# Performance work log

Measured on AMD Instinct MI355X. Metric: run time of the kernel, lower is better.

## Reference

```python
import jax, jax.numpy as jnp
from jax import lax
import numpy as np

EPS = 1e-6


def _conv1d_same(x, w, pad):
    # x: [B, 1, L], w: [1, 1, K]; XLA conv is cross-correlation, matching nn.Conv1d.
    return lax.conv_general_dilated(
        x, w, window_strides=(1,), padding=[(pad, pad)],
        dimension_numbers=("NCH", "OIH", "NCH"))


def setup_inputs() -> dict:
    key = jax.random.key(0)
    k_m, = jax.random.split(key, 1)
    B, L, K, NUM_LAYERS = 4096, 8192, 31, 10
    m = jax.random.uniform(k_m, (B, L), dtype=jnp.float32)
    # Gaussian instrument PSF (sigma=5), normalized to unit sum.
    xs = jnp.arange(K, dtype=jnp.float32) - (K - 1) / 2.0
    psf = jnp.exp(-(xs ** 2) / (2.0 * 5.0 ** 2))
    psf = psf / jnp.sum(psf)
    alpha = jnp.ones((NUM_LAYERS,), dtype=jnp.float32)
    return {"m": m, "psf": psf, "alpha": alpha}


def reference(m, psf, alpha):
    K = psf.shape[0]
    pad = (K - 1) // 2
    w = psf.reshape(1, 1, K)          # conv weight (PSF)
    w_flip = w[:, :, ::-1]             # flipped-PSF weight
    x = m[:, None, :]                  # [B, 1, L]
    s0 = jnp.full_like(x, 0.5)

    def step(s, a):
        s_conv = _conv1d_same(s, w, pad) + EPS
        ratio = x / s_conv
        correction = _conv1d_same(ratio, w_flip, pad) + EPS
        correction = jnp.maximum(correction, EPS)
        s = jnp.maximum(s * correction ** a, EPS)
        return s, None

    s, _ = lax.scan(step, s0, alpha)
    return s[:, 0, :]
```

## Files before the change

kernel.cpp:

```cpp
#include <hip/hip_runtime.h>
#include <math.h>

#define EPS     1e-6f
#define LROW    8192
#define NLAYER  10
#define NT      512

#define HBUF    16448
#define FRONTE  16
#define SCALE_F   2048.0f
#define INV_SCALE 4.8828125e-4f

typedef _Float16 half8  __attribute__((ext_vector_type(8)));
typedef __fp16   fp16x2 __attribute__((ext_vector_type(2)));
typedef float    f32x4  __attribute__((ext_vector_type(4)));

union H8U { uint4 u; half8 h; };
union H2U { fp16x2 h; unsigned int u; };

__device__ __forceinline__ half8 ldfrag(const char* p) {
    H8U w; w.u = *(const uint4*)(p); return w.h;
}

__device__ __forceinline__ int swz(int a) { return a ^ ((a >> 3) & 0x70); }

struct HL { _Float16 h, l; };
__device__ __forceinline__ HL fsplit(float v) {
    HL r;
    r.h = (_Float16)v;
    r.l = (_Float16)((v - (float)r.h) * SCALE_F);
    return r;
}

__device__ __forceinline__ float sgpr_f(float v) {
    return __int_as_float(__builtin_amdgcn_readfirstlane(__float_as_int(v)));
}

__device__ __forceinline__ void build_w(const float* wl, int am, int ag,
        half8& h01, half8& l01, half8& h2z, half8& l2z)
{
#pragma unroll
    for (int j = 0; j < 8; ++j) {
        const int k   = 8 * ag + j;
        const int i01 = k - am - 1;
        HL a = fsplit(wl[i01 + 16]);
        h01[j] = a.h; l01[j] = a.l;
        float v2 = 0.0f;
        if (k < 16) v2 = wl[31 + k - am + 16];
        HL b = fsplit(v2);
        h2z[j] = b.h; l2z[j] = b.l;
    }
}

__device__ __forceinline__ f32x4 conv_tile(const char* ph, const char* pl,
        int o01, int o2, half8 hA01, half8 lA01, half8 hA2, half8 lA2)
{
    half8 hS01 = ldfrag(ph + o01);
    half8 lS01 = ldfrag(pl + o01);
    half8 hS2  = ldfrag(ph + o2);
    half8 lS2  = ldfrag(pl + o2);
    f32x4 H  = {EPS, EPS, EPS, EPS};
    f32x4 L1 = {0.0f, 0.0f, 0.0f, 0.0f};
    f32x4 L2 = {0.0f, 0.0f, 0.0f, 0.0f};
    H  = __builtin_amdgcn_mfma_f32_16x16x32_f16(hA01, hS01, H,  0, 0, 0);
    H  = __builtin_amdgcn_mfma_f32_16x16x32_f16(hA2,  hS2,  H,  0, 0, 0);
    L1 = __builtin_amdgcn_mfma_f32_16x16x32_f16(lA01, hS01, L1, 0, 0, 0);
    L1 = __builtin_amdgcn_mfma_f32_16x16x32_f16(hA01, lS01, L1, 0, 0, 0);
    L2 = __builtin_amdgcn_mfma_f32_16x16x32_f16(lA2,  hS2,  L2, 0, 0, 0);
    L2 = __builtin_amdgcn_mfma_f32_16x16x32_f16(hA2,  lS2,  L2, 0, 0, 0);
    f32x4 r;
#pragma unroll
    for (int i = 0; i < 4; ++i) r[i] = fmaf(L1[i] + L2[i], INV_SCALE, H[i]);
    return r;
}

__global__ __launch_bounds__(NT, 4) void drl_kernel(
    const float* __restrict__ m,
    const float* __restrict__ psf,
    const float* __restrict__ alpha,
    float* __restrict__ out)
{
    __shared__ __align__(16) char lds[4 * HBUF + 256];
    char* SBh = lds;
    char* SBl = lds + HBUF;
    char* RBh = lds + 2 * HBUF;
    char* RBl = lds + 3 * HBUF;
    float* wl = (float*)(lds + 4 * HBUF);

    const int t    = threadIdx.x;
    const int lane = t & 63;
    const int wid  = t >> 6;
    const int am   = lane & 15;
    const int ag   = lane >> 4;
    const int row  = blockIdx.x;
    const float* mrow = m + (size_t)row * LROW;
    float*       orow = out + (size_t)row * LROW;

    {
        const uint4 z4 = make_uint4(0u, 0u, 0u, 0u);
        uint4* z = (uint4*)lds;
#pragma unroll
        for (int k = 0; k < 9; ++k) {
            int i = t + NT * k;
            if (i < 4112) z[i] = z4;
        }
        if (t < 64) wl[t] = (t >= 16 && t <= 46) ? psf[t - 16] : 0.0f;
    }
    __syncthreads();

    {
        const uint4 p5 = make_uint4(0x38003800u, 0x38003800u, 0x38003800u, 0x38003800u);
        int a = swz(32 + 32 * t);
        *(uint4*)(SBh + a)      = p5;
        *(uint4*)(SBh + a + 16) = p5;
    }
    __syncthreads();

    half8 hA01, lA01, hA2, lA2;
    build_w(wl, am, ag, hA01, lA01, hA2, lA2);

    const int n0 = 64 * wid;
    const int xoff = 16 * (n0 + am) + 4 * ag;
    float4 xr[4];
#pragma unroll
    for (int c = 0; c < 4; ++c)
        xr[c] = *(const float4*)(mrow + xoff + 256 * c);

    float sreg[16];
#pragma unroll
    for (int i = 0; i < 16; ++i) sreg[i] = 0.5f;

    int rb01[4], rb2[4], wbw[4];
#pragma unroll
    for (int c = 0; c < 4; ++c) {
        const int e01 = 16 * (n0 + am - 1) + 8 * ag       + FRONTE + 256 * c;
        const int e2  = 16 * (n0 + am + 1) + 8 * (ag & 1) + FRONTE + 256 * c;
        const int ew  = 16 * (n0 + am)     + 4 * ag       + FRONTE + 256 * c;
        rb01[c] = swz(2 * e01);
        rb2[c]  = swz(2 * e2);
        wbw[c]  = swz(2 * ew);
    }

#pragma unroll 1
    for (int layer = 0; layer < NLAYER; ++layer) {
        const float a = sgpr_f(alpha[layer]);

#pragma unroll
        for (int c = 0; c < 4; ++c) {
            f32x4 acc = conv_tile(SBh, SBl, rb01[c], rb2[c],
                                  hA01, lA01, hA2, lA2);
            const float4 xv = xr[c];
            float r0 = xv.x * __builtin_amdgcn_rcpf(acc[0]);
            float r1 = xv.y * __builtin_amdgcn_rcpf(acc[1]);
            float r2 = xv.z * __builtin_amdgcn_rcpf(acc[2]);
            float r3 = xv.w * __builtin_amdgcn_rcpf(acc[3]);
            H2U hA, hB, lA, lB;
            hA.h = __builtin_amdgcn_cvt_pkrtz(r0, r1);
            hB.h = __builtin_amdgcn_cvt_pkrtz(r2, r3);
            float d0 = (r0 - (float)hA.h.x) * SCALE_F;
            float d1 = (r1 - (float)hA.h.y) * SCALE_F;
            float d2 = (r2 - (float)hB.h.x) * SCALE_F;
            float d3 = (r3 - (float)hB.h.y) * SCALE_F;
            lA.h = __builtin_amdgcn_cvt_pkrtz(d0, d1);
            lB.h = __builtin_amdgcn_cvt_pkrtz(d2, d3);
            *(uint2*)(RBh + wbw[c]) = make_uint2(hA.u, hB.u);
            *(uint2*)(RBl + wbw[c]) = make_uint2(lA.u, lB.u);
        }
        __syncthreads();

#pragma unroll
        for (int c = 0; c < 4; ++c) {
            f32x4 acc = conv_tile(RBh, RBl, rb01[c], rb2[c],
                                  hA01, lA01, hA2, lA2);
            float c0 = fmaxf(acc[0], EPS);
            float c1 = fmaxf(acc[1], EPS);
            float c2 = fmaxf(acc[2], EPS);
            float c3 = fmaxf(acc[3], EPS);
            if (a != 1.0f) {
                c0 = powf(c0, a); c1 = powf(c1, a);
                c2 = powf(c2, a); c3 = powf(c3, a);
            }
            float s0 = fmaxf(sreg[4*c+0] * c0, EPS);
            float s1 = fmaxf(sreg[4*c+1] * c1, EPS);
            float s2 = fmaxf(sreg[4*c+2] * c2, EPS);
            float s3 = fmaxf(sreg[4*c+3] * c3, EPS);
            sreg[4*c+0] = s0; sreg[4*c+1] = s1;
            sreg[4*c+2] = s2; sreg[4*c+3] = s3;
            H2U hA, hB, lA, lB;
            hA.h = __builtin_amdgcn_cvt_pkrtz(s0, s1);
            hB.h = __builtin_amdgcn_cvt_pkrtz(s2, s3);
            float d0 = (s0 - (float)hA.h.x) * SCALE_F;
            float d1 = (s1 - (float)hA.h.y) * SCALE_F;
            float d2 = (s2 - (float)hB.h.x) * SCALE_F;
            float d3 = (s3 - (float)hB.h.y) * SCALE_F;
            lA.h = __builtin_amdgcn_cvt_pkrtz(d0, d1);
            lB.h = __builtin_amdgcn_cvt_pkrtz(d2, d3);
            *(uint2*)(SBh + wbw[c]) = make_uint2(hA.u, hB.u);
            *(uint2*)(SBl + wbw[c]) = make_uint2(lA.u, lB.u);
        }
        __syncthreads();
    }

#pragma unroll
    for (int c = 0; c < 4; ++c) {
        *(float4*)(orow + xoff + 256 * c) =
            make_float4(sreg[4*c], sreg[4*c+1], sreg[4*c+2], sreg[4*c+3]);
    }
}

extern "C" void kernel_launch(void* const* d_in, const int* in_sizes, int n_in,
                              void* d_out, int out_size, void* d_ws, size_t ws_size,
                              hipStream_t stream) {
    const float* m     = (const float*)d_in[0];
    const float* psf   = (const float*)d_in[1];
    const float* alpha = (const float*)d_in[2];
    float* out = (float*)d_out;
    const int B = in_sizes[0] / LROW;
    drl_kernel<<<dim3(B), dim3(NT), 0, stream>>>(m, psf, alpha, out);
}
```

Before: 426.8 us.

## Switch banded convolution from 16x16x32 to 32x32x16 MFMA tiles

Replaces the per-chunk 16x16x32 MFMA Toeplitz formulation (six MFMAs per 16x16 tile, split into 01 and 2 weight blocks) with 32x32x16 MFMAs. Each lane's column now covers 32 contiguous outputs, with four K-chunks of weight fragments. The LDS layout, read/write offsets and input/output indexing are reworked to match. The aim is to cut MFMA issue count and wasted zero-weight work per output. The cost is larger accumulators (three f32x16) and more weight-fragment registers, which may hurt occupancy.

```diff
diff --git a/kernel.cpp b/kernel.cpp
--- a/kernel.cpp
+++ b/kernel.cpp
@@ -7,13 +7,12 @@
 #define NT      512
 
 #define HBUF    16448
-#define FRONTE  16
 #define SCALE_F   2048.0f
 #define INV_SCALE 4.8828125e-4f
 
 typedef _Float16 half8  __attribute__((ext_vector_type(8)));
 typedef __fp16   fp16x2 __attribute__((ext_vector_type(2)));
-typedef float    f32x4  __attribute__((ext_vector_type(4)));
+typedef float    f32x16 __attribute__((ext_vector_type(16)));
 
 union H8U { uint4 u; half8 h; };
 union H2U { fp16x2 h; unsigned int u; };
@@ -36,62 +35,25 @@
     return __int_as_float(__builtin_amdgcn_readfirstlane(__float_as_int(v)));
 }
 
-__device__ __forceinline__ void build_w(const float* wl, int am, int ag,
-        half8& h01, half8& l01, half8& h2z, half8& l2z)
-{
-#pragma unroll
-    for (int j = 0; j < 8; ++j) {
-        const int k   = 8 * ag + j;
-        const int i01 = k - am - 1;
-        HL a = fsplit(wl[i01 + 16]);
-        h01[j] = a.h; l01[j] = a.l;
-        float v2 = 0.0f;
-        if (k < 16) v2 = wl[31 + k - am + 16];
-        HL b = fsplit(v2);
-        h2z[j] = b.h; l2z[j] = b.l;
-    }
-}
-
-__device__ __forceinline__ f32x4 conv_tile(const char* ph, const char* pl,
-        int o01, int o2, half8 hA01, half8 lA01, half8 hA2, half8 lA2)
-{
-    half8 hS01 = ldfrag(ph + o01);
-    half8 lS01 = ldfrag(pl + o01);
-    half8 hS2  = ldfrag(ph + o2);
-    half8 lS2  = ldfrag(pl + o2);
-    f32x4 H  = {EPS, EPS, EPS, EPS};
-    f32x4 L1 = {0.0f, 0.0f, 0.0f, 0.0f};
-    f32x4 L2 = {0.0f, 0.0f, 0.0f, 0.0f};
-    H  = __builtin_amdgcn_mfma_f32_16x16x32_f16(hA01, hS01, H,  0, 0, 0);
-    H  = __builtin_amdgcn_mfma_f32_16x16x32_f16(hA2,  hS2,  H,  0, 0, 0);
-    L1 = __builtin_amdgcn_mfma_f32_16x16x32_f16(lA01, hS01, L1, 0, 0, 0);
-    L1 = __builtin_amdgcn_mfma_f32_16x16x32_f16(hA01, lS01, L1, 0, 0, 0);
-    L2 = __builtin_amdgcn_mfma_f32_16x16x32_f16(lA2,  hS2,  L2, 0, 0, 0);
-    L2 = __builtin_amdgcn_mfma_f32_16x16x32_f16(hA2,  lS2,  L2, 0, 0, 0);
-    f32x4 r;
-#pragma unroll
-    for (int i = 0; i < 4; ++i) r[i] = fmaf(L1[i] + L2[i], INV_SCALE, H[i]);
-    return r;
-}
-
 __global__ __launch_bounds__(NT, 4) void drl_kernel(
     const float* __restrict__ m,
     const float* __restrict__ psf,
     const float* __restrict__ alpha,
     float* __restrict__ out)
 {
-    __shared__ __align__(16) char lds[4 * HBUF + 256];
+    __shared__ __align__(16) char lds[4 * HBUF + 384];
     char* SBh = lds;
     char* SBl = lds + HBUF;
     char* RBh = lds + 2 * HBUF;
     char* RBl = lds + 3 * HBUF;
-    float* wl = (float*)(lds + 4 * HBUF);
+    float* wl2 = (float*)(lds + 4 * HBUF);
 
     const int t    = threadIdx.x;
     const int lane = t & 63;
     const int wid  = t >> 6;
-    const int am   = lane & 15;
-    const int ag   = lane >> 4;
+    const int aj   = lane & 31;
+    const int h    = lane >> 5;
+    const int col  = 32 * wid + aj;
     const int row  = blockIdx.x;
     const float* mrow = m + (size_t)row * LROW;
     float*       orow = out + (size_t)row * LROW;
@@ -104,107 +66,136 @@
             int i = t + NT * k;
             if (i < 4112) z[i] = z4;
         }
-        if (t < 64) wl[t] = (t >= 16 && t <= 46) ? psf[t - 16] : 0.0f;
+        if (t < 96) wl2[t] = (t >= 32 && t <= 62) ? psf[t - 32] : 0.0f;
     }
     __syncthreads();
 
     {
         const uint4 p5 = make_uint4(0x38003800u, 0x38003800u, 0x38003800u, 0x38003800u);
-        int a = swz(32 + 32 * t);
-        *(uint4*)(SBh + a)      = p5;
-        *(uint4*)(SBh + a + 16) = p5;
+        int a0 = swz(32 * t + 32);
+        *(uint4*)(SBh + a0) = p5;
+        int a1 = swz(32 * t + 48);
+        *(uint4*)(SBh + a1) = p5;
     }
     __syncthreads();
 
-    half8 hA01, lA01, hA2, lA2;
-    build_w(wl, am, ag, hA01, lA01, hA2, lA2);
-
-    const int n0 = 64 * wid;
-    const int xoff = 16 * (n0 + am) + 4 * ag;
-    float4 xr[4];
-#pragma unroll
-    for (int c = 0; c < 4; ++c)
-        xr[c] = *(const float4*)(mrow + xoff + 256 * c);
+    half8 hA[4], lA[4];
+#pragma unroll
+    for (int c = 0; c < 4; ++c) {
+#pragma unroll
+        for (int j = 0; j < 8; ++j) {
+            HL w = fsplit(wl2[16 * c + 8 * h + j - aj + 31]);
+            hA[c][j] = w.h; lA[c][j] = w.l;
+        }
+    }
+
+    int rb[4], wb[4];
+#pragma unroll
+    for (int c = 0; c < 4; ++c) {
+        rb[c] = swz(64 * col + 32 * c + 16 * h);
+        wb[c] = swz(64 * col + 16 * c + 8 * h + 32);
+    }
+
+    float xr[16];
+#pragma unroll
+    for (int q = 0; q < 4; ++q) {
+        float4 v = *(const float4*)(mrow + 32 * col + 8 * q + 4 * h);
+        xr[4*q+0] = v.x; xr[4*q+1] = v.y; xr[4*q+2] = v.z; xr[4*q+3] = v.w;
+    }
 
     float sreg[16];
 #pragma unroll
     for (int i = 0; i < 16; ++i) sreg[i] = 0.5f;
-
-    int rb01[4], rb2[4], wbw[4];
-#pragma unroll
-    for (int c = 0; c < 4; ++c) {
-        const int e01 = 16 * (n0 + am - 1) + 8 * ag       + FRONTE + 256 * c;
-        const int e2  = 16 * (n0 + am + 1) + 8 * (ag & 1) + FRONTE + 256 * c;
-        const int ew  = 16 * (n0 + am)     + 4 * ag       + FRONTE + 256 * c;
-        rb01[c] = swz(2 * e01);
-        rb2[c]  = swz(2 * e2);
-        wbw[c]  = swz(2 * ew);
-    }
 
 #pragma unroll 1
     for (int layer = 0; layer < NLAYER; ++layer) {
-        const float a = sgpr_f(alpha[layer]);
-
-#pragma unroll
-        for (int c = 0; c < 4; ++c) {
-            f32x4 acc = conv_tile(SBh, SBl, rb01[c], rb2[c],
-                                  hA01, lA01, hA2, lA2);
-            const float4 xv = xr[c];
-            float r0 = xv.x * __builtin_amdgcn_rcpf(acc[0]);
-            float r1 = xv.y * __builtin_amdgcn_rcpf(acc[1]);
-            float r2 = xv.z * __builtin_amdgcn_rcpf(acc[2]);
-            float r3 = xv.w * __builtin_amdgcn_rcpf(acc[3]);
-            H2U hA, hB, lA, lB;
-            hA.h = __builtin_amdgcn_cvt_pkrtz(r0, r1);
-            hB.h = __builtin_amdgcn_cvt_pkrtz(r2, r3);
-            float d0 = (r0 - (float)hA.h.x) * SCALE_F;
-            float d1 = (r1 - (float)hA.h.y) * SCALE_F;
-            float d2 = (r2 - (float)hB.h.x) * SCALE_F;
-            float d3 = (r3 - (float)hB.h.y) * SCALE_F;
-            lA.h = __builtin_amdgcn_cvt_pkrtz(d0, d1);
-            lB.h = __builtin_amdgcn_cvt_pkrtz(d2, d3);
-            *(uint2*)(RBh + wbw[c]) = make_uint2(hA.u, hB.u);
-            *(uint2*)(RBl + wbw[c]) = make_uint2(lA.u, lB.u);
+        const float av = sgpr_f(alpha[layer]);
+
+        {
+            f32x16 H, L1, L2;
+#pragma unroll
+            for (int i = 0; i < 16; ++i) { H[i] = EPS; L1[i] = 0.0f; L2[i] = 0.0f; }
+#pragma unroll
+            for (int c = 0; c < 4; ++c) {
+                half8 hB = ldfrag(SBh + rb[c]);
+                half8 lB = ldfrag(SBl + rb[c]);
+                H  = __builtin_amdgcn_mfma_f32_32x32x16_f16(hA[c], hB, H,  0, 0, 0);
+                L1 = __builtin_amdgcn_mfma_f32_32x32x16_f16(lA[c], hB, L1, 0, 0, 0);
+                L2 = __builtin_amdgcn_mfma_f32_32x32x16_f16(hA[c], lB, L2, 0, 0, 0);
+            }
+#pragma unroll
+            for (int q = 0; q < 4; ++q) {
+                float a0 = fmaf(L1[4*q+0] + L2[4*q+0], INV_SCALE, H[4*q+0]);
+                float a1 = fmaf(L1[4*q+1] + L2[4*q+1], INV_SCALE, H[4*q+1]);
+                float a2 = fmaf(L1[4*q+2] + L2[4*q+2], INV_SCALE, H[4*q+2]);
+                float a3 = fmaf(L1[4*q+3] + L2[4*q+3], INV_SCALE, H[4*q+3]);
+                float r0 = xr[4*q+0] * __builtin_amdgcn_rcpf(a0);
+                float r1 = xr[4*q+1] * __builtin_amdgcn_rcpf(a1);
+                float r2 = xr[4*q+2] * __builtin_amdgcn_rcpf(a2);
+                float r3 = xr[4*q+3] * __builtin_amdgcn_rcpf(a3);
+                H2U hP, hQ, lP, lQ;
+                hP.h = __builtin_amdgcn_cvt_pkrtz(r0, r1);
+                hQ.h = __builtin_amdgcn_cvt_pkrtz(r2, r3);
+                float d0 = (r0 - (float)hP.h.x) * SCALE_F;
+                float d1 = (r1 - (float)hP.h.y) * SCALE_F;
+                float d2 = (r2 - (float)hQ.h.x) * SCALE_F;
+                float d3 = (r3 - (float)hQ.h.y) * SCALE_F;
+                lP.h = __builtin_amdgcn_cvt_pkrtz(d0, d1);
+                lQ.h = __builtin_amdgcn_cvt_pkrtz(d2, d3);
+                *(uint2*)(RBh + wb[q]) = make_uint2(hP.u, hQ.u);
+                *(uint2*)(RBl + wb[q]) = make_uint2(lP.u, lQ.u);
+            }
         }
         __syncthreads();
 
-#pragma unroll
-        for (int c = 0; c < 4; ++c) {
-            f32x4 acc = conv_tile(RBh, RBl, rb01[c], rb2[c],
-                                  hA01, lA01, hA2, lA2);
-            float c0 = fmaxf(acc[0], EPS);
-            float c1 = fmaxf(acc[1], EPS);
-            float c2 = fmaxf(acc[2], EPS);
-            float c3 = fmaxf(acc[3], EPS);
-            if (a != 1.0f) {
-                c0 = powf(c0, a); c1 = powf(c1, a);
-                c2 = powf(c2, a); c3 = powf(c3, a);
-            }
-            float s0 = fmaxf(sreg[4*c+0] * c0, EPS);
-            float s1 = fmaxf(sreg[4*c+1] * c1, EPS);
-            float s2 = fmaxf(sreg[4*c+2] * c2, EPS);
-            float s3 = fmaxf(sreg[4*c+3] * c3, EPS);
-            sreg[4*c+0] = s0; sreg[4*c+1] = s1;
-            sreg[4*c+2] = s2; sreg[4*c+3] = s3;
-            H2U hA, hB, lA, lB;
-            hA.h = __builtin_amdgcn_cvt_pkrtz(s0, s1);
-            hB.h = __builtin_amdgcn_cvt_pkrtz(s2, s3);
-            float d0 = (s0 - (float)hA.h.x) * SCALE_F;
-            float d1 = (s1 - (float)hA.h.y) * SCALE_F;
-            float d2 = (s2 - (float)hB.h.x) * SCALE_F;
-            float d3 = (s3 - (float)hB.h.y) * SCALE_F;
-            lA.h = __builtin_amdgcn_cvt_pkrtz(d0, d1);
-            lB.h = __builtin_amdgcn_cvt_pkrtz(d2, d3);
-            *(uint2*)(SBh + wbw[c]) = make_uint2(hA.u, hB.u);
-            *(uint2*)(SBl + wbw[c]) = make_uint2(lA.u, lB.u);
+        {
+            f32x16 H, L1, L2;
+#pragma unroll
+            for (int i = 0; i < 16; ++i) { H[i] = EPS; L1[i] = 0.0f; L2[i] = 0.0f; }
+#pragma unroll
+            for (int c = 0; c < 4; ++c) {
+                half8 hB = ldfrag(RBh + rb[c]);
+                half8 lB = ldfrag(RBl + rb[c]);
+                H  = __builtin_amdgcn_mfma_f32_32x32x16_f16(hA[c], hB, H,  0, 0, 0);
+                L1 = __builtin_amdgcn_mfma_f32_32x32x16_f16(lA[c], hB, L1, 0, 0, 0);
+                L2 = __builtin_amdgcn_mfma_f32_32x32x16_f16(hA[c], lB, L2, 0, 0, 0);
+            }
+#pragma unroll
+            for (int q = 0; q < 4; ++q) {
+                float c0 = fmaxf(fmaf(L1[4*q+0] + L2[4*q+0], INV_SCALE, H[4*q+0]), EPS);
+                float c1 = fmaxf(fmaf(L1[4*q+1] + L2[4*q+1], INV_SCALE, H[4*q+1]), EPS);
+                float c2 = fmaxf(fmaf(L1[4*q+2] + L2[4*q+2], INV_SCALE, H[4*q+2]), EPS);
+                float c3 = fmaxf(fmaf(L1[4*q+3] + L2[4*q+3], INV_SCALE, H[4*q+3]), EPS);
+                if (av != 1.0f) {
+                    c0 = powf(c0, av); c1 = powf(c1, av);
+                    c2 = powf(c2, av); c3 = powf(c3, av);
+                }
+                float s0 = fmaxf(sreg[4*q+0] * c0, EPS);
+                float s1 = fmaxf(sreg[4*q+1] * c1, EPS);
+                float s2 = fmaxf(sreg[4*q+2] * c2, EPS);
+                float s3 = fmaxf(sreg[4*q+3] * c3, EPS);
+                sreg[4*q+0] = s0; sreg[4*q+1] = s1;
+                sreg[4*q+2] = s2; sreg[4*q+3] = s3;
+                H2U hP, hQ, lP, lQ;
+                hP.h = __builtin_amdgcn_cvt_pkrtz(s0, s1);
+                hQ.h = __builtin_amdgcn_cvt_pkrtz(s2, s3);
+                float d0 = (s0 - (float)hP.h.x) * SCALE_F;
+                float d1 = (s1 - (float)hP.h.y) * SCALE_F;
+                float d2 = (s2 - (float)hQ.h.x) * SCALE_F;
+                float d3 = (s3 - (float)hQ.h.y) * SCALE_F;
+                lP.h = __builtin_amdgcn_cvt_pkrtz(d0, d1);
+                lQ.h = __builtin_amdgcn_cvt_pkrtz(d2, d3);
+                *(uint2*)(SBh + wb[q]) = make_uint2(hP.u, hQ.u);
+                *(uint2*)(SBl + wb[q]) = make_uint2(lP.u, lQ.u);
+            }
         }
         __syncthreads();
     }
 
 #pragma unroll
-    for (int c = 0; c < 4; ++c) {
-        *(float4*)(orow + xoff + 256 * c) =
-            make_float4(sreg[4*c], sreg[4*c+1], sreg[4*c+2], sreg[4*c+3]);
+    for (int q = 0; q < 4; ++q) {
+        *(float4*)(orow + 32 * col + 8 * q + 4 * h) =
+            make_float4(sreg[4*q+0], sreg[4*q+1], sreg[4*q+2], sreg[4*q+3]);
     }
 }
 
```

Result: slower. 692.3 us (+62.2%).
